# Kernel tuning notes

Measured on AMD Instinct MI355X. Metric: run time of the kernel, lower is better.

## Reference

```python
import jax, jax.numpy as jnp
import numpy as np
from jax import lax

HEADS = 8
DIM_HEAD = 64
EPS = 1e-5


def _rel_pos_indices(size):
    ar = np.arange(size)
    pos = np.stack(np.meshgrid(ar, ar, indexing='ij'), axis=-1).reshape(-1, 2)  # (n, 2)
    rel = pos[:, None, :] - pos[None, :, :] + size - 1                          # (n, n, 2)
    return rel[..., 0] * (2 * size - 1) + rel[..., 1]                           # (n, n)


def _dwconv(t, w, b):
    # depthwise 3x3, same padding; w: (C,1,3,3)
    y = lax.conv_general_dilated(t, w, (1, 1), 'SAME',
                                 feature_group_count=t.shape[1],
                                 dimension_numbers=('NCHW', 'OIHW', 'NCHW'))
    return y + b[None, :, None, None]


def setup_inputs() -> dict:
    key = jax.random.key(0)
    ks = jax.random.split(key, 8)
    B, C, S = 16, 512, 32
    inner = HEADS * DIM_HEAD
    return {
        'x': jax.random.normal(ks[0], (B, C, S, S), jnp.float32),
        'gamma': jnp.ones((1, C, 1, 1), jnp.float32),
        'w_qkv': jax.random.normal(ks[1], (inner * 3, C), jnp.float32) * 0.02,
        'dw_w_q': jax.random.normal(ks[2], (inner, 1, 3, 3), jnp.float32) * 0.1,
        'dw_b_q': jnp.zeros((inner,), jnp.float32),
        'dw_w_k': jax.random.normal(ks[3], (inner, 1, 3, 3), jnp.float32) * 0.1,
        'dw_b_k': jnp.zeros((inner,), jnp.float32),
        'dw_w_v': jax.random.normal(ks[4], (inner, 1, 3, 3), jnp.float32) * 0.1,
        'dw_b_v': jnp.zeros((inner,), jnp.float32),
        'w_out': jax.random.normal(ks[5], (C, inner), jnp.float32) * 0.02,
        'pos_emb': jax.random.normal(ks[6], ((2 * S - 1) ** 2, HEADS), jnp.float32) * 0.02,
    }


def reference(x, gamma, w_qkv, dw_w_q, dw_b_q, dw_w_k, dw_b_k, dw_w_v, dw_b_v, w_out, pos_emb):
    B, C, H, W = x.shape
    scale = DIM_HEAD ** -0.5

    # ChanLayerNorm over channel dim (biased variance)
    mean = jnp.mean(x, axis=1, keepdims=True)
    var = jnp.var(x, axis=1, keepdims=True)
    xn = (x - mean) * lax.rsqrt(var + EPS) * gamma

    # 1x1 conv to qkv
    qkv = jnp.einsum('bchw,oc->bohw', xn, w_qkv)
    q, k, v = jnp.split(qkv, 3, axis=1)

    # depthwise "primer" convs
    q = _dwconv(q, dw_w_q, dw_b_q)
    k = _dwconv(k, dw_w_k, dw_b_k)
    v = _dwconv(v, dw_w_v, dw_b_v)

    # b (h d) x y -> b h (x y) d
    def to_heads(t):
        return t.reshape(B, HEADS, DIM_HEAD, H * W).transpose(0, 1, 3, 2)
    q, k, v = to_heads(q), to_heads(k), to_heads(v)

    sim = jnp.einsum('bhid,bhjd->bhij', q * scale, k)

    # relative position bias (static index table)
    idx = _rel_pos_indices(H)               # (n, n) numpy, static
    bias = pos_emb[idx]                      # (n, n, heads)
    sim = sim + jnp.transpose(bias, (2, 0, 1))[None]

    attn = jax.nn.softmax(sim.astype(jnp.float32), axis=-1)
    out = jnp.einsum('bhij,bhjd->bhid', attn, v)

    # b h (x y) d -> b (h d) x y
    out = out.transpose(0, 1, 3, 2).reshape(B, HEADS * DIM_HEAD, H, W)
    return jnp.einsum('bchw,oc->bohw', out, w_out)
```

## Files before the change

### kernel.cpp

```cpp
#include <hip/hip_runtime.h>
#include <hip/hip_bf16.h>


typedef __attribute__((ext_vector_type(8))) short bf16x8;
typedef __attribute__((ext_vector_type(4))) float f32x4;
typedef __attribute__((ext_vector_type(8))) unsigned short ushort8;

#define HEADS 8
#define DHEAD 64
#define NB 16
#define CCH 512
#define NPOS 1024
#define QKV_CH 1536
#define INNER 512

static __device__ __forceinline__ unsigned short f2bf(float f) {
    unsigned u = __builtin_bit_cast(unsigned, f);
    unsigned r = (u + 0x7fffu + ((u >> 16) & 1u)) >> 16;
    return (unsigned short)r;
}
static __device__ __forceinline__ float bf2f(unsigned short h) {
    unsigned u = ((unsigned)h) << 16;
    return __builtin_bit_cast(float, u);
}

#define DPP_ROR(v, CTRL)                                                       \
    __builtin_bit_cast(float, __builtin_amdgcn_update_dpp(                     \
        0, __builtin_bit_cast(int, (v)), (CTRL), 0xF, 0xF, true))

#define GLOAD_LDS16(gp, lp)                                                    \
    __builtin_amdgcn_global_load_lds(                                          \
        (const __attribute__((address_space(1))) void*)(gp),                   \
        (__attribute__((address_space(3))) void*)(lp), 16, 0, 0)

__global__ void cvt_kernel(const float* __restrict__ wqkv, const float* __restrict__ wout,
                           unsigned short* __restrict__ wqkv_bf, unsigned short* __restrict__ wout_bf) {
    int i = blockIdx.x * 256 + threadIdx.x;
    if (i < QKV_CH * CCH) wqkv_bf[i] = f2bf(wqkv[i]);
    if (i < CCH * INNER) wout_bf[i] = f2bf(wout[i]);
}

__global__ __launch_bounds__(256) void ln_kernel(const float* __restrict__ x,
                                                 const float* __restrict__ gamma,
                                                 unsigned short* __restrict__ xn_t) {
    __shared__ __align__(16) float sX[CCH * 32];
    __shared__ float red[2][8][32];
    __shared__ float stat[2][32];
    const int b = blockIdx.x >> 5;
    const int p0 = (blockIdx.x & 31) * 32;
    const int tid = threadIdx.x, w = tid >> 6, lane = tid & 63;
    const float* xb = x + (size_t)b * CCH * NPOS;
#pragma unroll
    for (int i = 0; i < 16; ++i) {
        int destB = i * 4096 + w * 1024 + lane * 16;
        int c = destB >> 7;
        int colb = destB & 127;
        GLOAD_LDS16(xb + (size_t)c * NPOS + p0 + (colb >> 2), (char*)sX + i * 4096 + w * 1024);
    }
    __syncthreads();
    const int p = tid & 31, cg = tid >> 5;
    float s = 0.f, s2 = 0.f;
#pragma unroll 8
    for (int i = 0; i < 64; ++i) {
        float v = sX[(cg * 64 + i) * 32 + p];
        s += v; s2 += v * v;
    }
    red[0][cg][p] = s; red[1][cg][p] = s2;
    __syncthreads();
    if (tid < 32) {
        float ts = 0.f, t2 = 0.f;
#pragma unroll
        for (int g = 0; g < 8; ++g) { ts += red[0][g][tid]; t2 += red[1][g][tid]; }
        float mean = ts * (1.f / CCH);
        float var = t2 * (1.f / CCH) - mean * mean;
        stat[0][tid] = mean;
        stat[1][tid] = rsqrtf(var + 1e-5f);
    }
    __syncthreads();
    const float mean = stat[0][p], rs = stat[1][p];
    unsigned short* orow = xn_t + ((size_t)(b * NPOS + p0 + p)) * CCH + cg * 64;
#pragma unroll
    for (int c0 = 0; c0 < 64; c0 += 8) {
        ushort8 o;
#pragma unroll
        for (int j = 0; j < 8; ++j) {
            float v = sX[(cg * 64 + c0 + j) * 32 + p];
            o[j] = f2bf((v - mean) * rs * gamma[cg * 64 + c0 + j]);
        }
        *(ushort8*)(orow + c0) = o;
    }
}

template <typename TO>
__global__ __launch_bounds__(256) void gemm_bt(const unsigned short* __restrict__ A,
                                               const unsigned short* __restrict__ Bt,
                                               TO* __restrict__ Cc, int M, int N, int K) {
    __shared__ __align__(16) unsigned short sA[128 * 64];
    __shared__ __align__(16) unsigned short sB[128 * 64];
    const int tid = threadIdx.x;
    const int w = tid >> 6, lane = tid & 63;
    const int wr = w >> 1, wc = w & 1;
    const int fr = lane & 15, fg = lane >> 4;
    const int m0 = blockIdx.y * 128, n0 = blockIdx.x * 128;
    const unsigned short* Ab = A + (size_t)m0 * K;
    const unsigned short* Bb = Bt + (size_t)blockIdx.z * N * K + (size_t)n0 * K;

    f32x4 acc[4][4];
#pragma unroll
    for (int i = 0; i < 4; ++i)
#pragma unroll
        for (int j = 0; j < 4; ++j) acc[i][j] = {0.f, 0.f, 0.f, 0.f};

    for (int k0 = 0; k0 < K; k0 += 64) {
#pragma unroll
        for (int i = 0; i < 4; ++i) {
            int e = i * 2048 + tid * 8;
            int row = e >> 6, col = e & 63;
            GLOAD_LDS16(Ab + (size_t)row * K + k0 + col, sA + i * 2048 + w * 512);
            GLOAD_LDS16(Bb + (size_t)row * K + k0 + col, sB + i * 2048 + w * 512);
        }
        __syncthreads();
#pragma unroll
        for (int ks = 0; ks < 2; ++ks) {
            bf16x8 aF[4], bF[4];
#pragma unroll
            for (int mm = 0; mm < 4; ++mm)
                aF[mm] = *(const bf16x8*)(sA + (wr * 64 + mm * 16 + fr) * 64 + ks * 32 + fg * 8);
#pragma unroll
            for (int nn = 0; nn < 4; ++nn)
                bF[nn] = *(const bf16x8*)(sB + (wc * 64 + nn * 16 + fr) * 64 + ks * 32 + fg * 8);
#pragma unroll
            for (int mm = 0; mm < 4; ++mm)
#pragma unroll
                for (int nn = 0; nn < 4; ++nn)
                    acc[mm][nn] = __builtin_amdgcn_mfma_f32_16x16x32_bf16(aF[mm], bF[nn], acc[mm][nn], 0, 0, 0);
        }
        __syncthreads();
    }
    TO* Cb = Cc + (size_t)blockIdx.z * M * N;
#pragma unroll
    for (int mm = 0; mm < 4; ++mm) {
#pragma unroll
        for (int j = 0; j < 4; ++j) {
            int r = m0 + wr * 64 + mm * 16 + fg * 4 + j;
#pragma unroll
            for (int nn = 0; nn < 4; ++nn) {
                int c = n0 + wc * 64 + nn * 16 + fr;
                float v = acc[mm][nn][j];
                if constexpr (sizeof(TO) == 2) Cb[(size_t)r * N + c] = f2bf(v);
                else Cb[(size_t)r * N + c] = v;
            }
        }
    }
}

__global__ __launch_bounds__(256) void dwconv_kernel(const unsigned short* __restrict__ qkv,
                              const float* __restrict__ wq, const float* __restrict__ bq,
                              const float* __restrict__ wk, const float* __restrict__ bk,
                              const float* __restrict__ wv, const float* __restrict__ bv,
                              unsigned short* __restrict__ qa, unsigned short* __restrict__ ka,
                              unsigned short* __restrict__ vt) {
    __shared__ __align__(16) unsigned short sIn[64 * 320];
    __shared__ float wS[64 * 9];
    __shared__ float bS[64];
    const int yt = blockIdx.x & 3;
    const int hw = blockIdx.x >> 2;
    const int b = blockIdx.y;
    const int which = hw >> 3, h = hw & 7;
    const int y0 = yt * 8;
    const float* wsel = which == 0 ? wq : which == 1 ? wk : wv;
    const float* bsel = which == 0 ? bq : which == 1 ? bk : bv;
    const int ocbase = which * 512 + h * 64;
    const int tid = threadIdx.x;

    for (int i = tid; i < 576; i += 256) wS[i] = wsel[(size_t)h * 64 * 9 + i];
    if (tid < 64) bS[tid] = bsel[h * 64 + tid];

    const unsigned short* src = qkv + ((size_t)b * QKV_CH + ocbase) * NPOS;
#pragma unroll
    for (int it = 0; it < 10; ++it) {
        int idx = it * 256 + tid;
        int ch = idx / 40, rem = idx % 40;
        int j = rem >> 2, q = rem & 3;
        int yy = y0 - 1 + j;
        ushort8 v = {0, 0, 0, 0, 0, 0, 0, 0};
        if (yy >= 0 && yy < 32) v = *(const ushort8*)(src + (size_t)ch * NPOS + yy * 32 + q * 8);
        *(ushort8*)(sIn + ch * 320 + j * 32 + q * 8) = v;
    }
    __syncthreads();

    const int r = tid >> 5, xx = tid & 31;
    const float scale = which == 0 ? 0.125f : 1.f;
#pragma unroll
    for (int chunk = 0; chunk < 8; ++chunk) {
        ushort8 ob;
#pragma unroll
        for (int dd = 0; dd < 8; ++dd) {
            int d = chunk * 8 + dd;
            float acc = bS[d];
            const float* w9 = wS + d * 9;
#pragma unroll
            for (int dy = 0; dy < 3; ++dy) {
                const unsigned short* rowp = sIn + d * 320 + (r + dy) * 32;
#pragma unroll
                for (int dx = 0; dx < 3; ++dx) {
                    int xc = xx + dx - 1;
                    if (xc >= 0 && xc < 32) acc += w9[dy * 3 + dx] * bf2f(rowp[xc]);
                }
            }
            ob[dd] = f2bf(acc * scale);
        }
        if (which == 2) {
#pragma unroll
            for (int dd = 0; dd < 8; ++dd)
                vt[((size_t)(b * HEADS + h) * DHEAD + chunk * 8 + dd) * NPOS + y0 * 32 + tid] = ob[dd];
        } else {
            unsigned short* dst = (which == 0 ? qa : ka) +
                ((size_t)(b * HEADS + h) * NPOS + y0 * 32 + tid) * DHEAD + chunk * 8;
            *(ushort8*)dst = ob;
        }
    }
}

__global__ __launch_bounds__(256) void attn_kernel(const unsigned short* __restrict__ qa,
                                                   const unsigned short* __restrict__ ka,
                                                   const unsigned short* __restrict__ vt,
                                                   const float* __restrict__ pos_emb,
                                                   unsigned short* __restrict__ att_t) {
    __shared__ float bias_s[3969];
    __shared__ __align__(16) unsigned short kT[64 * 64];
    __shared__ __align__(16) unsigned short vT[64 * 64];
    __shared__ __align__(16) unsigned short pS[4 * 16 * 64];
    const int tid = threadIdx.x, w = tid >> 6, lane = tid & 63;
    const int fr = lane & 15, fg = lane >> 4;
    const int qb = blockIdx.x, h = blockIdx.y, b = blockIdx.z;
    const int bh = b * HEADS + h;
    const unsigned short* qbase = qa + (size_t)bh * NPOS * DHEAD;
    const unsigned short* kbase = ka + (size_t)bh * NPOS * DHEAD;
    const unsigned short* vbase = vt + (size_t)bh * DHEAD * NPOS;

    for (int i = tid; i < 3969; i += 256) bias_s[i] = pos_emb[i * HEADS + h];

    const int i0 = qb * 64 + w * 16;
    bf16x8 aQ[2];
#pragma unroll
    for (int ks = 0; ks < 2; ++ks)
        aQ[ks] = *(const bf16x8*)(qbase + (size_t)(i0 + fr) * DHEAD + ks * 32 + fg * 8);

    const int dB0 = w * 1024 + lane * 16;
    const int dB1 = 4096 + w * 1024 + lane * 16;
    const int row0 = dB0 >> 7, row1 = dB1 >> 7;
    const int col0 = ((dB0 & 127) ^ ((row0 & 7) << 4)) >> 1;
    const int col1 = ((dB1 & 127) ^ ((row1 & 7) << 4)) >> 1;

    bf16x8 rk0 = *(const bf16x8*)(kbase + (size_t)row0 * DHEAD + col0);
    bf16x8 rk1 = *(const bf16x8*)(kbase + (size_t)row1 * DHEAD + col1);
    bf16x8 rv0 = *(const bf16x8*)(vbase + (size_t)row0 * NPOS + col0);
    bf16x8 rv1 = *(const bf16x8*)(vbase + (size_t)row1 * NPOS + col1);

    float m[4], l[4];
    f32x4 o[4];
#pragma unroll
    for (int j = 0; j < 4; ++j) { m[j] = -1e30f; l[j] = 0.f; }
#pragma unroll
    for (int dn = 0; dn < 4; ++dn) o[dn] = {0.f, 0.f, 0.f, 0.f};

    __syncthreads();

    for (int t = 0; t < 16; ++t) {
        const int kv0 = t * 64;
        *(bf16x8*)((char*)kT + dB0) = rk0;
        *(bf16x8*)((char*)kT + dB1) = rk1;
        *(bf16x8*)((char*)vT + dB0) = rv0;
        *(bf16x8*)((char*)vT + dB1) = rv1;
        if (t < 15) {
            const int kv1 = kv0 + 64;
            rk0 = *(const bf16x8*)(kbase + (size_t)(kv1 + row0) * DHEAD + col0);
            rk1 = *(const bf16x8*)(kbase + (size_t)(kv1 + row1) * DHEAD + col1);
            rv0 = *(const bf16x8*)(vbase + (size_t)row0 * NPOS + kv1 + col0);
            rv1 = *(const bf16x8*)(vbase + (size_t)row1 * NPOS + kv1 + col1);
        }
        __syncthreads();

        f32x4 s[4];
#pragma unroll
        for (int nn = 0; nn < 4; ++nn) s[nn] = {0.f, 0.f, 0.f, 0.f};
#pragma unroll
        for (int ks = 0; ks < 2; ++ks) {
#pragma unroll
            for (int nn = 0; nn < 4; ++nn) {
                unsigned kb = (unsigned)(((nn * 16 + fr) * 64 + ks * 32 + fg * 8) * 2);
                kb ^= ((kb >> 7) & 7) << 4;
                bf16x8 bK = *(const bf16x8*)((const char*)kT + kb);
                s[nn] = __builtin_amdgcn_mfma_f32_16x16x32_bf16(aQ[ks], bK, s[nn], 0, 0, 0);
            }
        }
        float pm[4];
#pragma unroll
        for (int j = 0; j < 4; ++j) {
            int iglob = i0 + fg * 4 + j;
            int yi = iglob >> 5, xi = iglob & 31;
            float tm = -1e30f;
#pragma unroll
            for (int nn = 0; nn < 4; ++nn) {
                int jglob = kv0 + nn * 16 + fr;
                int yj = jglob >> 5, xj = jglob & 31;
                int bidx = (yi - yj + 31) * 63 + (xi - xj + 31);
                s[nn][j] += bias_s[bidx];
                tm = fmaxf(tm, s[nn][j]);
            }
            tm = fmaxf(tm, DPP_ROR(tm, 0x121));
            tm = fmaxf(tm, DPP_ROR(tm, 0x122));
            tm = fmaxf(tm, DPP_ROR(tm, 0x124));
            tm = fmaxf(tm, DPP_ROR(tm, 0x128));
            pm[j] = fmaxf(m[j], tm);
        }
#pragma unroll
        for (int j = 0; j < 4; ++j) {
            float alpha = __expf(m[j] - pm[j]);
            float rsum = 0.f;
#pragma unroll
            for (int nn = 0; nn < 4; ++nn) {
                float pv = __expf(s[nn][j] - pm[j]);
                s[nn][j] = pv;
                rsum += pv;
            }
            rsum += DPP_ROR(rsum, 0x121);
            rsum += DPP_ROR(rsum, 0x122);
            rsum += DPP_ROR(rsum, 0x124);
            rsum += DPP_ROR(rsum, 0x128);
            l[j] = l[j] * alpha + rsum;
            m[j] = pm[j];
#pragma unroll
            for (int dn = 0; dn < 4; ++dn) o[dn][j] *= alpha;
        }
#pragma unroll
        for (int j = 0; j < 4; ++j) {
            int rrow = fg * 4 + j;
#pragma unroll
            for (int nn = 0; nn < 4; ++nn) {
                unsigned pb = (unsigned)((w * 16 + rrow) * 128 + (nn * 16 + fr) * 2);
                pb ^= ((pb >> 7) & 7) << 4;
                *(unsigned short*)((char*)pS + pb) = f2bf(s[nn][j]);
            }
        }
#pragma unroll
        for (int ks = 0; ks < 2; ++ks) {
            unsigned pb = (unsigned)((w * 16 + fr) * 128 + (ks * 32 + fg * 8) * 2);
            pb ^= ((pb >> 7) & 7) << 4;
            bf16x8 aP = *(const bf16x8*)((const char*)pS + pb);
#pragma unroll
            for (int dn = 0; dn < 4; ++dn) {
                unsigned vb = (unsigned)(((dn * 16 + fr) * 64 + ks * 32 + fg * 8) * 2);
                vb ^= ((vb >> 7) & 7) << 4;
                bf16x8 bV = *(const bf16x8*)((const char*)vT + vb);
                o[dn] = __builtin_amdgcn_mfma_f32_16x16x32_bf16(aP, bV, o[dn], 0, 0, 0);
            }
        }
        __syncthreads();
    }
#pragma unroll
    for (int j = 0; j < 4; ++j) {
        float inv = 1.f / l[j];
        int iglob = i0 + fg * 4 + j;
        unsigned short* orow = att_t + ((size_t)b * NPOS + iglob) * INNER + h * DHEAD;
#pragma unroll
        for (int dn = 0; dn < 4; ++dn) orow[dn * 16 + fr] = f2bf(o[dn][j] * inv);
    }
}

extern "C" void kernel_launch(void* const* d_in, const int* in_sizes, int n_in,
                              void* d_out, int out_size, void* d_ws, size_t ws_size,
                              hipStream_t stream) {
    const float* x      = (const float*)d_in[0];
    const float* gamma  = (const float*)d_in[1];
    const float* w_qkv  = (const float*)d_in[2];
    const float* dw_w_q = (const float*)d_in[3];
    const float* dw_b_q = (const float*)d_in[4];
    const float* dw_w_k = (const float*)d_in[5];
    const float* dw_b_k = (const float*)d_in[6];
    const float* dw_w_v = (const float*)d_in[7];
    const float* dw_b_v = (const float*)d_in[8];
    const float* w_out  = (const float*)d_in[9];
    const float* pos_emb = (const float*)d_in[10];
    float* out = (float*)d_out;
    char* ws = (char*)d_ws;

    const size_t MB = 1024 * 1024;
    unsigned short* wqkv_bf = (unsigned short*)(ws + 0);
    unsigned short* wout_bf = (unsigned short*)(ws + 1536 * 512 * 2);
    unsigned short* xn_t    = (unsigned short*)(ws + 2 * MB);
    unsigned short* qkv     = (unsigned short*)(ws + 18 * MB);
    unsigned short* qa      = (unsigned short*)(ws + 66 * MB);
    unsigned short* kb      = (unsigned short*)(ws + 82 * MB);
    unsigned short* vt      = (unsigned short*)(ws + 2 * MB);
    unsigned short* att_t   = (unsigned short*)(ws + 18 * MB);

    cvt_kernel<<<dim3(3072), dim3(256), 0, stream>>>(w_qkv, w_out, wqkv_bf, wout_bf);
    ln_kernel<<<dim3(512), dim3(256), 0, stream>>>(x, gamma, xn_t);
    gemm_bt<unsigned short><<<dim3(8, 12, 16), dim3(256), 0, stream>>>(wqkv_bf, xn_t, qkv, 1536, 1024, 512);
    dwconv_kernel<<<dim3(96, 16), dim3(256), 0, stream>>>(qkv, dw_w_q, dw_b_q, dw_w_k, dw_b_k,
                                                          dw_w_v, dw_b_v, qa, kb, vt);
    attn_kernel<<<dim3(16, 8, 16), dim3(256), 0, stream>>>(qa, kb, vt, pos_emb, att_t);
    gemm_bt<float><<<dim3(8, 4, 16), dim3(256), 0, stream>>>(wout_bf, att_t, out, 512, 1024, 512);
}
```

Measured before the change: 242.2 us.

## Restructure dwconv with channel-interleaved padded LDS tile and split channels across blocks

The depthwise conv kernel now stores its input tile in shared memory with 8 channels interleaved per pixel and zero-padded x borders. Each thread reads one 16-byte vector per tap and accumulates 8 channels at once, which removes the per-tap boundary branches and scalar LDS reads. Each block now handles 32 channels instead of 64, so the grid doubles, which should improve occupancy and parallelism. The cost is a scattered 2-byte LDS write pattern during the load phase, which may cause bank conflicts.

```diff
diff --git a/kernel.cpp b/kernel.cpp
--- a/kernel.cpp
+++ b/kernel.cpp
@@ -160,63 +160,77 @@
                               const float* __restrict__ wv, const float* __restrict__ bv,
                               unsigned short* __restrict__ qa, unsigned short* __restrict__ ka,
                               unsigned short* __restrict__ vt) {
-    __shared__ __align__(16) unsigned short sIn[64 * 320];
-    __shared__ float wS[64 * 9];
-    __shared__ float bS[64];
+    __shared__ __align__(16) unsigned short sIn[4 * 10 * 34 * 8];
+    __shared__ __align__(16) float wS[9][32];
+    __shared__ float bS[32];
     const int yt = blockIdx.x & 3;
-    const int hw = blockIdx.x >> 2;
+    const int chalf = (blockIdx.x >> 2) & 1;
+    const int hw = blockIdx.x >> 3;
+    const int which = hw >> 3, h = hw & 7;
     const int b = blockIdx.y;
-    const int which = hw >> 3, h = hw & 7;
     const int y0 = yt * 8;
     const float* wsel = which == 0 ? wq : which == 1 ? wk : wv;
     const float* bsel = which == 0 ? bq : which == 1 ? bk : bv;
-    const int ocbase = which * 512 + h * 64;
+    const int ocbase = which * 512 + h * 64 + chalf * 32;
     const int tid = threadIdx.x;
 
-    for (int i = tid; i < 576; i += 256) wS[i] = wsel[(size_t)h * 64 * 9 + i];
-    if (tid < 64) bS[tid] = bsel[h * 64 + tid];
+    for (int i = tid; i < 288; i += 256) {
+        int dloc = i / 9, k = i % 9;
+        wS[k][dloc] = wsel[(size_t)(h * 64 + chalf * 32 + dloc) * 9 + k];
+    }
+    if (tid < 32) bS[tid] = bsel[h * 64 + chalf * 32 + tid];
 
     const unsigned short* src = qkv + ((size_t)b * QKV_CH + ocbase) * NPOS;
 #pragma unroll
-    for (int it = 0; it < 10; ++it) {
+    for (int it = 0; it < 5; ++it) {
         int idx = it * 256 + tid;
         int ch = idx / 40, rem = idx % 40;
         int j = rem >> 2, q = rem & 3;
         int yy = y0 - 1 + j;
         ushort8 v = {0, 0, 0, 0, 0, 0, 0, 0};
         if (yy >= 0 && yy < 32) v = *(const ushort8*)(src + (size_t)ch * NPOS + yy * 32 + q * 8);
-        *(ushort8*)(sIn + ch * 320 + j * 32 + q * 8) = v;
+        unsigned short* d0 = sIn + (((ch >> 3) * 10 + j) * 34 + (q * 8 + 1)) * 8 + (ch & 7);
+#pragma unroll
+        for (int e = 0; e < 8; ++e) d0[e * 8] = v[e];
+    }
+    {
+        ushort8 z = {0, 0, 0, 0, 0, 0, 0, 0};
+        for (int i = tid; i < 80; i += 256) {
+            int c = i / 20, rr = i % 20;
+            int j = rr >> 1, side = rr & 1;
+            *(ushort8*)(sIn + ((c * 10 + j) * 34 + (side ? 33 : 0)) * 8) = z;
+        }
     }
     __syncthreads();
 
     const int r = tid >> 5, xx = tid & 31;
     const float scale = which == 0 ? 0.125f : 1.f;
 #pragma unroll
-    for (int chunk = 0; chunk < 8; ++chunk) {
+    for (int c = 0; c < 4; ++c) {
+        float acc[8];
+#pragma unroll
+        for (int dd = 0; dd < 8; ++dd) acc[dd] = bS[c * 8 + dd];
+#pragma unroll
+        for (int dy = 0; dy < 3; ++dy) {
+#pragma unroll
+            for (int dx = 0; dx < 3; ++dx) {
+                ushort8 v = *(const ushort8*)(sIn + ((c * 10 + r + dy) * 34 + xx + dx) * 8);
+#pragma unroll
+                for (int dd = 0; dd < 8; ++dd)
+                    acc[dd] += wS[dy * 3 + dx][c * 8 + dd] * bf2f(v[dd]);
+            }
+        }
         ushort8 ob;
 #pragma unroll
-        for (int dd = 0; dd < 8; ++dd) {
-            int d = chunk * 8 + dd;
-            float acc = bS[d];
-            const float* w9 = wS + d * 9;
-#pragma unroll
-            for (int dy = 0; dy < 3; ++dy) {
-                const unsigned short* rowp = sIn + d * 320 + (r + dy) * 32;
-#pragma unroll
-                for (int dx = 0; dx < 3; ++dx) {
-                    int xc = xx + dx - 1;
-                    if (xc >= 0 && xc < 32) acc += w9[dy * 3 + dx] * bf2f(rowp[xc]);
-                }
-            }
-            ob[dd] = f2bf(acc * scale);
-        }
+        for (int dd = 0; dd < 8; ++dd) ob[dd] = f2bf(acc[dd] * scale);
+        const int p = (y0 + r) * 32 + xx;
         if (which == 2) {
 #pragma unroll
             for (int dd = 0; dd < 8; ++dd)
-                vt[((size_t)(b * HEADS + h) * DHEAD + chunk * 8 + dd) * NPOS + y0 * 32 + tid] = ob[dd];
+                vt[((size_t)(b * HEADS + h) * DHEAD + chalf * 32 + c * 8 + dd) * NPOS + p] = ob[dd];
         } else {
             unsigned short* dst = (which == 0 ? qa : ka) +
-                ((size_t)(b * HEADS + h) * NPOS + y0 * 32 + tid) * DHEAD + chunk * 8;
+                ((size_t)(b * HEADS + h) * NPOS + p) * DHEAD + chalf * 32 + c * 8;
             *(ushort8*)dst = ob;
         }
     }
@@ -399,8 +413,8 @@
     cvt_kernel<<<dim3(3072), dim3(256), 0, stream>>>(w_qkv, w_out, wqkv_bf, wout_bf);
     ln_kernel<<<dim3(512), dim3(256), 0, stream>>>(x, gamma, xn_t);
     gemm_bt<unsigned short><<<dim3(8, 12, 16), dim3(256), 0, stream>>>(wqkv_bf, xn_t, qkv, 1536, 1024, 512);
-    dwconv_kernel<<<dim3(96, 16), dim3(256), 0, stream>>>(qkv, dw_w_q, dw_b_q, dw_w_k, dw_b_k,
-                                                          dw_w_v, dw_b_v, qa, kb, vt);
+    dwconv_kernel<<<dim3(192, 16), dim3(256), 0, stream>>>(qkv, dw_w_q, dw_b_q, dw_w_k, dw_b_k,
+                                                           dw_w_v, dw_b_v, qa, kb, vt);
     attn_kernel<<<dim3(16, 8, 16), dim3(256), 0, stream>>>(qa, kb, vt, pos_emb, att_t);
     gemm_bt<float><<<dim3(8, 4, 16), dim3(256), 0, stream>>>(wout_bf, att_t, out, 512, 1024, 512);
 }
```

Result: faster. 211.2 us (-12.8%).
